# Optimization experiments

Measured on AMD Instinct MI355X. Metric: run time of the kernel, lower is better.

## Reference

```python
import jax, jax.numpy as jnp
import numpy as np

P = 30000      # nodes (WSI patches)
DIN = 1536     # input feature dim
DOUT = 256     # output dim
HEADS = 2
C = DOUT // HEADS  # per-head channels = 128
E = 320000     # edges (before self-loops)
NEG_SLOPE = 0.2


def setup_inputs() -> dict:
    key = jax.random.key(0)
    ks = jax.random.split(key, 12)
    g = lambda k, shape: jax.random.normal(k, shape, jnp.float32) * 0.02
    return {
        "x": jax.random.normal(ks[0], (P, DIN), jnp.float32),
        "edge_index": jax.random.randint(ks[1], (2, E), 0, P),
        "W1l": g(ks[2], (DIN, DOUT)), "b1l": jnp.zeros((DOUT,), jnp.float32),
        "W1r": g(ks[3], (DIN, DOUT)), "b1r": jnp.zeros((DOUT,), jnp.float32),
        "att1": g(ks[4], (HEADS, C)), "bias1": jnp.zeros((DOUT,), jnp.float32),
        "W2l": g(ks[5], (DOUT, DOUT)), "b2l": jnp.zeros((DOUT,), jnp.float32),
        "W2r": g(ks[6], (DOUT, DOUT)), "b2r": jnp.zeros((DOUT,), jnp.float32),
        "att2": g(ks[7], (HEADS, C)), "bias2": jnp.zeros((DOUT,), jnp.float32),
        "ln1_g": jnp.ones((DOUT,), jnp.float32), "ln1_b": jnp.zeros((DOUT,), jnp.float32),
        "ln2_g": jnp.ones((DOUT,), jnp.float32), "ln2_b": jnp.zeros((DOUT,), jnp.float32),
        "resW": g(ks[8], (DIN, DOUT)), "resb": jnp.zeros((DOUT,), jnp.float32),
    }


def layer_norm(h, g, b, eps=1e-5):
    mu = h.mean(-1, keepdims=True)
    var = ((h - mu) ** 2).mean(-1, keepdims=True)
    return (h - mu) * jax.lax.rsqrt(var + eps) * g + b


def gatv2(x, src, dst, Wl, bl, Wr, br, att, bias):
    # PyG GATv2Conv: lin_l on source j, lin_r on target i,
    # e_ij = att . LeakyReLU(xl[j] + xr[i]); softmax over incoming edges of i;
    # out_i = sum_j alpha_ij * xl[j]  (heads concatenated) + bias.
    n = x.shape[0]
    xl = (x @ Wl + bl).reshape(n, HEADS, C)
    xr = (x @ Wr + br).reshape(n, HEADS, C)
    m = jax.nn.leaky_relu(xl[src] + xr[dst], NEG_SLOPE)      # (Etot, H, C)
    e = jnp.einsum('ehc,hc->eh', m, att)                     # (Etot, H)
    emax = jax.ops.segment_max(e, dst, num_segments=n)       # stable segment softmax
    ex = jnp.exp(e - emax[dst])
    den = jax.ops.segment_sum(ex, dst, num_segments=n)
    alpha = ex / den[dst]                                    # (Etot, H)
    out = jax.ops.segment_sum(xl[src] * alpha[..., None], dst, num_segments=n)
    return out.reshape(n, HEADS * C) + bias


def reference(x, edge_index, W1l, b1l, W1r, b1r, att1, bias1,
              W2l, b2l, W2r, b2r, att2, bias2,
              ln1_g, ln1_b, ln2_g, ln2_b, resW, resb):
    loops = jnp.arange(P)
    src = jnp.concatenate([edge_index[0], loops])  # add self loops
    dst = jnp.concatenate([edge_index[1], loops])

    h1 = gatv2(x, src, dst, W1l, b1l, W1r, b1r, att1, bias1)
    h1 = jax.nn.elu(layer_norm(h1, ln1_g, ln1_b)) + (x @ resW + resb)

    h2 = gatv2(h1, src, dst, W2l, b2l, W2r, b2r, att2, bias2)
    h2 = jax.nn.elu(layer_norm(h2, ln2_g, ln2_b)) + h2 * 0 + h1 + (h2 - h1) * 0 if False else jax.nn.elu(layer_norm(h2, ln2_g, ln2_b)) + h1
    # JK-max combine of the two layer outputs
    return jnp.maximum(h1, h2)
```

## Files before the change

### kernel.cpp

```cpp
#include <hip/hip_runtime.h>
#include <math.h>

#define P_NODES 30000
#define DIN_    1536
#define DOUT_   256
#define E_EDGES 320000
#define ET      (E_EDGES + P_NODES)
#define NEG     0.2f

typedef float  f32x4  __attribute__((ext_vector_type(4)));
typedef __bf16 bf16x8 __attribute__((ext_vector_type(8)));
typedef __bf16 bf16x4 __attribute__((ext_vector_type(4)));

__global__ __launch_bounds__(256)
void prep_w1(const float* __restrict__ W1l, const float* __restrict__ W1r,
             const float* __restrict__ resW, __bf16* __restrict__ WT1)
{
    int idx = blockIdx.x * 256 + threadIdx.x;
    if (idx >= DIN_ * 192) return;
    int k = idx / 192;
    int n0 = (idx - k * 192) * 4;
    const float* src; int col;
    if (n0 < 256)      { src = W1l;  col = n0; }
    else if (n0 < 512) { src = W1r;  col = n0 - 256; }
    else               { src = resW; col = n0 - 512; }
    f32x4 v = *(const f32x4*)(src + (size_t)k * DOUT_ + col);
    #pragma unroll
    for (int j = 0; j < 4; ++j)
        WT1[(size_t)(n0 + j) * DIN_ + k] = (__bf16)v[j];
}

__global__ __launch_bounds__(256)
void prep_w2(const float* __restrict__ W2l, const float* __restrict__ W2r,
             __bf16* __restrict__ WT2)
{
    int idx = blockIdx.x * 256 + threadIdx.x;
    if (idx >= 256 * 128) return;
    int k = idx / 128;
    int n0 = (idx - k * 128) * 4;
    const float* src; int col;
    if (n0 < 256) { src = W2l; col = n0; }
    else          { src = W2r; col = n0 - 256; }
    f32x4 v = *(const f32x4*)(src + (size_t)k * DOUT_ + col);
    #pragma unroll
    for (int j = 0; j < 4; ++j)
        WT2[(size_t)(n0 + j) * DOUT_ + k] = (__bf16)v[j];
}

__global__ void prep_bias(const float* b1l, const float* b1r, const float* resb,
                          const float* b2l, const float* b2r,
                          float* B1, float* B2)
{
    int t = threadIdx.x;
    if (t < 256)      B1[t] = b1l[t];
    else if (t < 512) B1[t] = b1r[t - 256];
    else if (t < 768) B1[t] = resb[t - 512];
    if (t < 256)      B2[t] = b2l[t];
    else if (t < 512) B2[t] = b2r[t - 256];
}

__global__ void init_deg(int* deg)
{
    int i = blockIdx.x * 256 + threadIdx.x;
    if (i < P_NODES) deg[i] = 1;
}

__global__ void hist_kernel(const int* __restrict__ dst, int* __restrict__ deg)
{
    int e = blockIdx.x * 256 + threadIdx.x;
    if (e < E_EDGES) atomicAdd(&deg[dst[e]], 1);
}

__global__ __launch_bounds__(1024)
void scan_kernel(const int* __restrict__ deg, int* __restrict__ offs, int* __restrict__ pos)
{
    __shared__ int sb[1024];
    const int t = threadIdx.x;
    const int base = t * 30;
    int ldv[30];
    int lsum = 0;
    #pragma unroll
    for (int i = 0; i < 30; ++i) {
        int idx = base + i;
        int v = (idx < P_NODES) ? deg[idx] : 0;
        ldv[i] = v; lsum += v;
    }
    sb[t] = lsum; __syncthreads();
    for (int off = 1; off < 1024; off <<= 1) {
        int v = (t >= off) ? sb[t - off] : 0;
        __syncthreads();
        sb[t] += v;
        __syncthreads();
    }
    int excl = sb[t] - lsum;
    #pragma unroll
    for (int i = 0; i < 30; ++i) {
        int idx = base + i;
        if (idx < P_NODES) { offs[idx] = excl; pos[idx] = excl; excl += ldv[i]; }
    }
    if (t == 0) offs[P_NODES] = ET;
}

__global__ void scatter_kernel(const int* __restrict__ ei, int* __restrict__ pos,
                               int* __restrict__ srcs)
{
    int tgt = blockIdx.x * 256 + threadIdx.x;
    if (tgt < E_EDGES) {
        int s = ei[tgt];
        int d = ei[E_EDGES + tgt];
        int p = atomicAdd(&pos[d], 1);
        srcs[p] = s;
    } else if (tgt < ET) {
        int i = tgt - E_EDGES;
        int p = atomicAdd(&pos[i], 1);
        srcs[p] = i;
    }
}

template<bool A_F32>
__global__ __launch_bounds__(256)
void gemm_kernel(const void* __restrict__ Av, const __bf16* __restrict__ WT,
                 const float* __restrict__ bias, float* __restrict__ C,
                 int M, int N, int K, int ntiles)
{
    __shared__ __align__(16) __bf16 As[128 * 32];
    __shared__ __align__(16) __bf16 Bs[128 * 32];

    const int bid = blockIdx.x;
    const int mt = bid / ntiles, nt = bid - mt * ntiles;
    const int grow = mt * 128, gcol = nt * 128;
    const int t = threadIdx.x;
    const int lane = t & 63, wave = t >> 6;
    const int wr = wave >> 1, wc = wave & 1;
    const int fr = lane & 15, kg = lane >> 4;

    const int srow = t >> 1, shalf = t & 1;
    int arow = grow + srow; if (arow > M - 1) arow = M - 1;
    const int swz = (srow >> 1) & 3;
    const int g0 = shalf * 2;

    f32x4 acc[4][4] = {};

    for (int k0 = 0; k0 < K; k0 += 32) {
        bf16x8 a0, a1, b0, b1;
        if constexpr (A_F32) {
            const float* ap = (const float*)Av + (size_t)arow * K + k0 + shalf * 16;
            f32x4 v0 = *(const f32x4*)(ap + 0);
            f32x4 v1 = *(const f32x4*)(ap + 4);
            f32x4 v2 = *(const f32x4*)(ap + 8);
            f32x4 v3 = *(const f32x4*)(ap + 12);
            #pragma unroll
            for (int j = 0; j < 4; ++j) {
                a0[j] = (__bf16)v0[j]; a0[j + 4] = (__bf16)v1[j];
                a1[j] = (__bf16)v2[j]; a1[j + 4] = (__bf16)v3[j];
            }
        } else {
            const __bf16* ap = (const __bf16*)Av + (size_t)arow * K + k0 + shalf * 16;
            a0 = *(const bf16x8*)(ap);
            a1 = *(const bf16x8*)(ap + 8);
        }
        {
            const __bf16* bp = WT + (size_t)(gcol + srow) * K + k0 + shalf * 16;
            b0 = *(const bf16x8*)(bp);
            b1 = *(const bf16x8*)(bp + 8);
        }
        __syncthreads();
        *(bf16x8*)&As[srow * 32 + ((g0    ) ^ swz) * 8] = a0;
        *(bf16x8*)&As[srow * 32 + ((g0 + 1) ^ swz) * 8] = a1;
        *(bf16x8*)&Bs[srow * 32 + ((g0    ) ^ swz) * 8] = b0;
        *(bf16x8*)&Bs[srow * 32 + ((g0 + 1) ^ swz) * 8] = b1;
        __syncthreads();

        bf16x8 af[4], bf[4];
        #pragma unroll
        for (int mi = 0; mi < 4; ++mi) {
            int r = wr * 64 + mi * 16 + fr;
            af[mi] = *(const bf16x8*)&As[r * 32 + (kg ^ ((r >> 1) & 3)) * 8];
        }
        #pragma unroll
        for (int ni = 0; ni < 4; ++ni) {
            int r = wc * 64 + ni * 16 + fr;
            bf[ni] = *(const bf16x8*)&Bs[r * 32 + (kg ^ ((r >> 1) & 3)) * 8];
        }
        #pragma unroll
        for (int mi = 0; mi < 4; ++mi)
            #pragma unroll
            for (int ni = 0; ni < 4; ++ni)
                acc[mi][ni] = __builtin_amdgcn_mfma_f32_16x16x32_bf16(af[mi], bf[ni], acc[mi][ni], 0, 0, 0);
    }

    #pragma unroll
    for (int mi = 0; mi < 4; ++mi) {
        #pragma unroll
        for (int ni = 0; ni < 4; ++ni) {
            int col = gcol + wc * 64 + ni * 16 + fr;
            float bv = bias[col];
            #pragma unroll
            for (int j = 0; j < 4; ++j) {
                int row = grow + wr * 64 + mi * 16 + kg * 4 + j;
                if (row < M) C[(size_t)row * N + col] = acc[mi][ni][j] + bv;
            }
        }
    }
}

__global__ __launch_bounds__(256)
void gat_kernel(const float* __restrict__ XLXR, int ld,
                const int* __restrict__ offs, const int* __restrict__ srcs,
                const float* __restrict__ att, const float* __restrict__ bias,
                float* __restrict__ out)
{
    const int node = blockIdx.x * 4 + (threadIdx.x >> 6);
    const int lane = threadIdx.x & 63;
    const int c0 = lane * 4;
    f32x4 xr = *(const f32x4*)(XLXR + (size_t)node * ld + 256 + c0);
    f32x4 at = *(const f32x4*)(att + c0);
    f32x4 acc = {0.f, 0.f, 0.f, 0.f};
    float m = -INFINITY, den = 0.f;
    const int e1 = offs[node + 1];
    for (int e = offs[node]; e < e1; ++e) {
        int s = srcs[e];
        f32x4 xl = *(const f32x4*)(XLXR + (size_t)s * ld + c0);
        float p = 0.f;
        #pragma unroll
        for (int j = 0; j < 4; ++j) {
            float tt = xl[j] + xr[j];
            float lr = tt > 0.f ? tt : NEG * tt;
            p = fmaf(at[j], lr, p);
        }
        #pragma unroll
        for (int w = 1; w < 32; w <<= 1) p += __shfl_xor(p, w, 32);
        float nm = fmaxf(m, p);
        float sc = __expf(m - nm);
        float wv = __expf(p - nm);
        den = den * sc + wv;
        #pragma unroll
        for (int j = 0; j < 4; ++j) acc[j] = acc[j] * sc + wv * xl[j];
        m = nm;
    }
    float inv = 1.f / den;
    f32x4 o;
    #pragma unroll
    for (int j = 0; j < 4; ++j) o[j] = acc[j] * inv + bias[c0 + j];
    *(f32x4*)(out + (size_t)node * DOUT_ + c0) = o;
}

__global__ __launch_bounds__(256)
void h1_kernel(const float* __restrict__ GAT, const float* __restrict__ RESbase, int resld,
               const float* __restrict__ g, const float* __restrict__ b,
               float* __restrict__ H1, __bf16* __restrict__ H1B)
{
    const int node = blockIdx.x * 4 + (threadIdx.x >> 6);
    const int lane = threadIdx.x & 63;
    const int c0 = lane * 4;
    f32x4 h = *(const f32x4*)(GAT + (size_t)node * DOUT_ + c0);
    float s = h[0] + h[1] + h[2] + h[3];
    #pragma unroll
    for (int w = 1; w < 64; w <<= 1) s += __shfl_xor(s, w, 64);
    float mu = s * (1.f / DOUT_);
    f32x4 d; float sq = 0.f;
    #pragma unroll
    for (int j = 0; j < 4; ++j) { d[j] = h[j] - mu; sq += d[j] * d[j]; }
    #pragma unroll
    for (int w = 1; w < 64; w <<= 1) sq += __shfl_xor(sq, w, 64);
    float rs = rsqrtf(sq * (1.f / DOUT_) + 1e-5f);
    f32x4 res = *(const f32x4*)(RESbase + (size_t)node * resld + c0);
    f32x4 o; bf16x4 hb;
    #pragma unroll
    for (int j = 0; j < 4; ++j) {
        float y = d[j] * rs * g[c0 + j] + b[c0 + j];
        float e = y > 0.f ? y : __expf(y) - 1.f;
        o[j] = e + res[j];
        hb[j] = (__bf16)o[j];
    }
    *(f32x4*)(H1 + (size_t)node * DOUT_ + c0) = o;
    *(bf16x4*)(H1B + (size_t)node * DOUT_ + c0) = hb;
}

__global__ __launch_bounds__(256)
void final_kernel(const float* __restrict__ GAT2, const float* __restrict__ H1,
                  const float* __restrict__ g, const float* __restrict__ b,
                  float* __restrict__ out)
{
    const int node = blockIdx.x * 4 + (threadIdx.x >> 6);
    const int lane = threadIdx.x & 63;
    const int c0 = lane * 4;
    f32x4 h = *(const f32x4*)(GAT2 + (size_t)node * DOUT_ + c0);
    float s = h[0] + h[1] + h[2] + h[3];
    #pragma unroll
    for (int w = 1; w < 64; w <<= 1) s += __shfl_xor(s, w, 64);
    float mu = s * (1.f / DOUT_);
    f32x4 d; float sq = 0.f;
    #pragma unroll
    for (int j = 0; j < 4; ++j) { d[j] = h[j] - mu; sq += d[j] * d[j]; }
    #pragma unroll
    for (int w = 1; w < 64; w <<= 1) sq += __shfl_xor(sq, w, 64);
    float rs = rsqrtf(sq * (1.f / DOUT_) + 1e-5f);
    f32x4 h1v = *(const f32x4*)(H1 + (size_t)node * DOUT_ + c0);
    f32x4 o;
    #pragma unroll
    for (int j = 0; j < 4; ++j) {
        float y = d[j] * rs * g[c0 + j] + b[c0 + j];
        float e = y > 0.f ? y : __expf(y) - 1.f;
        float h2 = e + h1v[j];
        o[j] = fmaxf(h1v[j], h2);
    }
    *(f32x4*)(out + (size_t)node * DOUT_ + c0) = o;
}

extern "C" void kernel_launch(void* const* d_in, const int* in_sizes, int n_in,
                              void* d_out, int out_size, void* d_ws, size_t ws_size,
                              hipStream_t stream)
{
    const float* x     = (const float*)d_in[0];
    const int*   ei    = (const int*)d_in[1];
    const float* W1l   = (const float*)d_in[2];
    const float* b1l   = (const float*)d_in[3];
    const float* W1r   = (const float*)d_in[4];
    const float* b1r   = (const float*)d_in[5];
    const float* att1  = (const float*)d_in[6];
    const float* bias1 = (const float*)d_in[7];
    const float* W2l   = (const float*)d_in[8];
    const float* b2l   = (const float*)d_in[9];
    const float* W2r   = (const float*)d_in[10];
    const float* b2r   = (const float*)d_in[11];
    const float* att2  = (const float*)d_in[12];
    const float* bias2 = (const float*)d_in[13];
    const float* ln1g  = (const float*)d_in[14];
    const float* ln1b  = (const float*)d_in[15];
    const float* ln2g  = (const float*)d_in[16];
    const float* ln2b  = (const float*)d_in[17];
    const float* resW  = (const float*)d_in[18];
    const float* resb  = (const float*)d_in[19];
    float* out = (float*)d_out;

    char* w = (char*)d_ws;
    auto alloc = [&](size_t bytes) {
        char* r = w;
        w += (bytes + 255) & ~(size_t)255;
        return r;
    };
    float*  C     = (float*)alloc((size_t)P_NODES * 768 * 4);
    float*  GAT   = (float*)alloc((size_t)P_NODES * 256 * 4);
    float*  H1    = (float*)alloc((size_t)P_NODES * 256 * 4);
    __bf16* H1B   = (__bf16*)alloc((size_t)P_NODES * 256 * 2);
    __bf16* WT1   = (__bf16*)alloc((size_t)768 * DIN_ * 2);
    __bf16* WT2   = (__bf16*)alloc((size_t)512 * DOUT_ * 2);
    float*  BIAS1 = (float*)alloc(768 * 4);
    float*  BIAS2 = (float*)alloc(512 * 4);
    int*    deg   = (int*)alloc((size_t)P_NODES * 4);
    int*    offs  = (int*)alloc((size_t)(P_NODES + 1) * 4);
    int*    pos   = (int*)alloc((size_t)(P_NODES + 1) * 4);
    int*    srcs  = (int*)alloc((size_t)ET * 4);

    prep_w1<<<(DIN_ * 192 + 255) / 256, 256, 0, stream>>>(W1l, W1r, resW, WT1);
    prep_w2<<<(256 * 128 + 255) / 256, 256, 0, stream>>>(W2l, W2r, WT2);
    prep_bias<<<1, 1024, 0, stream>>>(b1l, b1r, resb, b2l, b2r, BIAS1, BIAS2);
    init_deg<<<(P_NODES + 255) / 256, 256, 0, stream>>>(deg);
    hist_kernel<<<(E_EDGES + 255) / 256, 256, 0, stream>>>(ei + E_EDGES, deg);
    scan_kernel<<<1, 1024, 0, stream>>>(deg, offs, pos);
    scatter_kernel<<<(ET + 255) / 256, 256, 0, stream>>>(ei, pos, srcs);

    const int mtiles = (P_NODES + 127) / 128;

    gemm_kernel<true><<<mtiles * 6, 256, 0, stream>>>(x, WT1, BIAS1, C, P_NODES, 768, DIN_, 6);
    gat_kernel<<<P_NODES / 4, 256, 0, stream>>>(C, 768, offs, srcs, att1, bias1, GAT);
    h1_kernel<<<P_NODES / 4, 256, 0, stream>>>(GAT, C + 512, 768, ln1g, ln1b, H1, H1B);

    gemm_kernel<false><<<mtiles * 4, 256, 0, stream>>>(H1B, WT2, BIAS2, C, P_NODES, 512, DOUT_, 4);
    gat_kernel<<<P_NODES / 4, 256, 0, stream>>>(C, 512, offs, srcs, att2, bias2, GAT);
    final_kernel<<<P_NODES / 4, 256, 0, stream>>>(GAT, H1, ln2g, ln2b, out);
}
```

Before: 732.7 us.

## Pre-cast x to swizzled bf16, use direct global-to-LDS loads, store XL/XR in bf16

A separate pass casts x to bf16 in a padded, XOR-swizzled layout, and the weights and H1B are written with the same swizzle. The GEMM can then fill LDS with global_load_lds DMA over a 64-wide K tile and no in-register conversion. The GEMM now writes the XL/XR projections as bf16 and only the residual as fp32, which halves the bytes the gather-heavy GAT kernels read per edge. Costs are an extra full pass over x, lower precision in the attention inputs, and workspace buffers aliased inside the XB region.

```diff
diff --git a/kernel.cpp b/kernel.cpp
--- a/kernel.cpp
+++ b/kernel.cpp
@@ -2,6 +2,7 @@
 #include <math.h>
 
 #define P_NODES 30000
+#define P_PAD   30080
 #define DIN_    1536
 #define DOUT_   256
 #define E_EDGES 320000
@@ -11,6 +12,31 @@
 typedef float  f32x4  __attribute__((ext_vector_type(4)));
 typedef __bf16 bf16x8 __attribute__((ext_vector_type(8)));
 typedef __bf16 bf16x4 __attribute__((ext_vector_type(4)));
+
+__device__ __forceinline__ int swz_col(int c, int row) {
+    return (c & ~63) | ((((c >> 3) ^ row) & 7) << 3) | (c & 7);
+}
+
+__global__ __launch_bounds__(256)
+void cast_x(const float* __restrict__ x, __bf16* __restrict__ XB)
+{
+    int idx = blockIdx.x * 256 + threadIdx.x;
+    if (idx >= P_PAD * 192) return;
+    int row = idx / 192;
+    int c = (idx - row * 192) * 8;
+    int cs = swz_col(c, row);
+    bf16x8 o;
+    if (row < P_NODES) {
+        f32x4 v0 = *(const f32x4*)(x + (size_t)row * DIN_ + c);
+        f32x4 v1 = *(const f32x4*)(x + (size_t)row * DIN_ + c + 4);
+        #pragma unroll
+        for (int j = 0; j < 4; ++j) { o[j] = (__bf16)v0[j]; o[j + 4] = (__bf16)v1[j]; }
+    } else {
+        #pragma unroll
+        for (int j = 0; j < 8; ++j) o[j] = (__bf16)0.f;
+    }
+    *(bf16x8*)(XB + (size_t)row * DIN_ + cs) = o;
+}
 
 __global__ __launch_bounds__(256)
 void prep_w1(const float* __restrict__ W1l, const float* __restrict__ W1r,
@@ -26,8 +52,10 @@
     else               { src = resW; col = n0 - 512; }
     f32x4 v = *(const f32x4*)(src + (size_t)k * DOUT_ + col);
     #pragma unroll
-    for (int j = 0; j < 4; ++j)
-        WT1[(size_t)(n0 + j) * DIN_ + k] = (__bf16)v[j];
+    for (int j = 0; j < 4; ++j) {
+        int n = n0 + j;
+        WT1[(size_t)n * DIN_ + swz_col(k, n)] = (__bf16)v[j];
+    }
 }
 
 __global__ __launch_bounds__(256)
@@ -43,8 +71,10 @@
     else          { src = W2r; col = n0 - 256; }
     f32x4 v = *(const f32x4*)(src + (size_t)k * DOUT_ + col);
     #pragma unroll
-    for (int j = 0; j < 4; ++j)
-        WT2[(size_t)(n0 + j) * DOUT_ + k] = (__bf16)v[j];
+    for (int j = 0; j < 4; ++j) {
+        int n = n0 + j;
+        WT2[(size_t)n * DOUT_ + swz_col(k, n)] = (__bf16)v[j];
+    }
 }
 
 __global__ void prep_bias(const float* b1l, const float* b1r, const float* resb,
@@ -117,14 +147,15 @@
     }
 }
 
-template<bool A_F32>
-__global__ __launch_bounds__(256)
-void gemm_kernel(const void* __restrict__ Av, const __bf16* __restrict__ WT,
-                 const float* __restrict__ bias, float* __restrict__ C,
+template<int EPI>
+__global__ __launch_bounds__(256)
+void gemm_kernel(const __bf16* __restrict__ A, const __bf16* __restrict__ WT,
+                 const float* __restrict__ bias,
+                 __bf16* __restrict__ Cb, float* __restrict__ Cf,
                  int M, int N, int K, int ntiles)
 {
-    __shared__ __align__(16) __bf16 As[128 * 32];
-    __shared__ __align__(16) __bf16 Bs[128 * 32];
+    __shared__ __align__(16) __bf16 As[128 * 64];
+    __shared__ __align__(16) __bf16 Bs[128 * 64];
 
     const int bid = blockIdx.x;
     const int mt = bid / ntiles, nt = bid - mt * ntiles;
@@ -133,60 +164,44 @@
     const int lane = t & 63, wave = t >> 6;
     const int wr = wave >> 1, wc = wave & 1;
     const int fr = lane & 15, kg = lane >> 4;
-
-    const int srow = t >> 1, shalf = t & 1;
-    int arow = grow + srow; if (arow > M - 1) arow = M - 1;
-    const int swz = (srow >> 1) & 3;
-    const int g0 = shalf * 2;
+    const int frs = fr & 7;
+
+    const __bf16* agp = A  + (size_t)(grow + (t >> 3)) * K + (t & 7) * 8;
+    const __bf16* bgp = WT + (size_t)(gcol + (t >> 3)) * K + (t & 7) * 8;
+    const size_t rstep = (size_t)32 * K;
+    char* lA = (char*)As + wave * 1024;
+    char* lB = (char*)Bs + wave * 1024;
 
     f32x4 acc[4][4] = {};
 
-    for (int k0 = 0; k0 < K; k0 += 32) {
-        bf16x8 a0, a1, b0, b1;
-        if constexpr (A_F32) {
-            const float* ap = (const float*)Av + (size_t)arow * K + k0 + shalf * 16;
-            f32x4 v0 = *(const f32x4*)(ap + 0);
-            f32x4 v1 = *(const f32x4*)(ap + 4);
-            f32x4 v2 = *(const f32x4*)(ap + 8);
-            f32x4 v3 = *(const f32x4*)(ap + 12);
-            #pragma unroll
-            for (int j = 0; j < 4; ++j) {
-                a0[j] = (__bf16)v0[j]; a0[j + 4] = (__bf16)v1[j];
-                a1[j] = (__bf16)v2[j]; a1[j + 4] = (__bf16)v3[j];
-            }
-        } else {
-            const __bf16* ap = (const __bf16*)Av + (size_t)arow * K + k0 + shalf * 16;
-            a0 = *(const bf16x8*)(ap);
-            a1 = *(const bf16x8*)(ap + 8);
-        }
-        {
-            const __bf16* bp = WT + (size_t)(gcol + srow) * K + k0 + shalf * 16;
-            b0 = *(const bf16x8*)(bp);
-            b1 = *(const bf16x8*)(bp + 8);
+    for (int k0 = 0; k0 < K; k0 += 64) {
+        __syncthreads();
+        #pragma unroll
+        for (int i = 0; i < 4; ++i) {
+            __builtin_amdgcn_global_load_lds(
+                (const __attribute__((address_space(1))) void*)(agp + i * rstep + k0),
+                (__attribute__((address_space(3))) void*)(lA + i * 4096), 16, 0, 0);
+            __builtin_amdgcn_global_load_lds(
+                (const __attribute__((address_space(1))) void*)(bgp + i * rstep + k0),
+                (__attribute__((address_space(3))) void*)(lB + i * 4096), 16, 0, 0);
         }
         __syncthreads();
-        *(bf16x8*)&As[srow * 32 + ((g0    ) ^ swz) * 8] = a0;
-        *(bf16x8*)&As[srow * 32 + ((g0 + 1) ^ swz) * 8] = a1;
-        *(bf16x8*)&Bs[srow * 32 + ((g0    ) ^ swz) * 8] = b0;
-        *(bf16x8*)&Bs[srow * 32 + ((g0 + 1) ^ swz) * 8] = b1;
-        __syncthreads();
-
-        bf16x8 af[4], bf[4];
-        #pragma unroll
-        for (int mi = 0; mi < 4; ++mi) {
-            int r = wr * 64 + mi * 16 + fr;
-            af[mi] = *(const bf16x8*)&As[r * 32 + (kg ^ ((r >> 1) & 3)) * 8];
-        }
-        #pragma unroll
-        for (int ni = 0; ni < 4; ++ni) {
-            int r = wc * 64 + ni * 16 + fr;
-            bf[ni] = *(const bf16x8*)&Bs[r * 32 + (kg ^ ((r >> 1) & 3)) * 8];
-        }
-        #pragma unroll
-        for (int mi = 0; mi < 4; ++mi)
+
+        #pragma unroll
+        for (int ks = 0; ks < 2; ++ks) {
+            bf16x8 af[4], bv[4];
+            #pragma unroll
+            for (int mi = 0; mi < 4; ++mi)
+                af[mi] = *(const bf16x8*)&As[(wr * 64 + mi * 16 + fr) * 64 + (((ks * 4 + kg) ^ frs)) * 8];
             #pragma unroll
             for (int ni = 0; ni < 4; ++ni)
-                acc[mi][ni] = __builtin_amdgcn_mfma_f32_16x16x32_bf16(af[mi], bf[ni], acc[mi][ni], 0, 0, 0);
+                bv[ni] = *(const bf16x8*)&Bs[(wc * 64 + ni * 16 + fr) * 64 + (((ks * 4 + kg) ^ frs)) * 8];
+            #pragma unroll
+            for (int mi = 0; mi < 4; ++mi)
+                #pragma unroll
+                for (int ni = 0; ni < 4; ++ni)
+                    acc[mi][ni] = __builtin_amdgcn_mfma_f32_16x16x32_bf16(af[mi], bv[ni], acc[mi][ni], 0, 0, 0);
+        }
     }
 
     #pragma unroll
@@ -194,18 +209,26 @@
         #pragma unroll
         for (int ni = 0; ni < 4; ++ni) {
             int col = gcol + wc * 64 + ni * 16 + fr;
-            float bv = bias[col];
+            float bvv = bias[col];
             #pragma unroll
             for (int j = 0; j < 4; ++j) {
                 int row = grow + wr * 64 + mi * 16 + kg * 4 + j;
-                if (row < M) C[(size_t)row * N + col] = acc[mi][ni][j] + bv;
+                if (row < M) {
+                    float v = acc[mi][ni][j] + bvv;
+                    if (EPI == 0) {
+                        if (col < 512) Cb[(size_t)row * 512 + col] = (__bf16)v;
+                        else           Cf[(size_t)row * 256 + col - 512] = v;
+                    } else {
+                        Cb[(size_t)row * 512 + col] = (__bf16)v;
+                    }
+                }
             }
         }
     }
 }
 
 __global__ __launch_bounds__(256)
-void gat_kernel(const float* __restrict__ XLXR, int ld,
+void gat_kernel(const __bf16* __restrict__ XLXR,
                 const int* __restrict__ offs, const int* __restrict__ srcs,
                 const float* __restrict__ att, const float* __restrict__ bias,
                 float* __restrict__ out)
@@ -213,17 +236,21 @@
     const int node = blockIdx.x * 4 + (threadIdx.x >> 6);
     const int lane = threadIdx.x & 63;
     const int c0 = lane * 4;
-    f32x4 xr = *(const f32x4*)(XLXR + (size_t)node * ld + 256 + c0);
-    f32x4 at = *(const f32x4*)(att + c0);
+    bf16x4 xrb = *(const bf16x4*)(XLXR + (size_t)node * 512 + 256 + c0);
+    f32x4 xr, at = *(const f32x4*)(att + c0);
+    #pragma unroll
+    for (int j = 0; j < 4; ++j) xr[j] = (float)xrb[j];
     f32x4 acc = {0.f, 0.f, 0.f, 0.f};
     float m = -INFINITY, den = 0.f;
     const int e1 = offs[node + 1];
     for (int e = offs[node]; e < e1; ++e) {
         int s = srcs[e];
-        f32x4 xl = *(const f32x4*)(XLXR + (size_t)s * ld + c0);
+        bf16x4 xlb = *(const bf16x4*)(XLXR + (size_t)s * 512 + c0);
+        f32x4 xl;
         float p = 0.f;
         #pragma unroll
         for (int j = 0; j < 4; ++j) {
+            xl[j] = (float)xlb[j];
             float tt = xl[j] + xr[j];
             float lr = tt > 0.f ? tt : NEG * tt;
             p = fmaf(at[j], lr, p);
@@ -246,13 +273,21 @@
 }
 
 __global__ __launch_bounds__(256)
-void h1_kernel(const float* __restrict__ GAT, const float* __restrict__ RESbase, int resld,
+void h1_kernel(const float* __restrict__ GAT, const float* __restrict__ RES,
                const float* __restrict__ g, const float* __restrict__ b,
                float* __restrict__ H1, __bf16* __restrict__ H1B)
 {
     const int node = blockIdx.x * 4 + (threadIdx.x >> 6);
     const int lane = threadIdx.x & 63;
     const int c0 = lane * 4;
+    const int cs = swz_col(c0, node);
+    if (node >= P_NODES) {
+        bf16x4 z; 
+        #pragma unroll
+        for (int j = 0; j < 4; ++j) z[j] = (__bf16)0.f;
+        *(bf16x4*)(H1B + (size_t)node * DOUT_ + cs) = z;
+        return;
+    }
     f32x4 h = *(const f32x4*)(GAT + (size_t)node * DOUT_ + c0);
     float s = h[0] + h[1] + h[2] + h[3];
     #pragma unroll
@@ -264,7 +299,7 @@
     #pragma unroll
     for (int w = 1; w < 64; w <<= 1) sq += __shfl_xor(sq, w, 64);
     float rs = rsqrtf(sq * (1.f / DOUT_) + 1e-5f);
-    f32x4 res = *(const f32x4*)(RESbase + (size_t)node * resld + c0);
+    f32x4 res = *(const f32x4*)(RES + (size_t)node * DOUT_ + c0);
     f32x4 o; bf16x4 hb;
     #pragma unroll
     for (int j = 0; j < 4; ++j) {
@@ -274,7 +309,7 @@
         hb[j] = (__bf16)o[j];
     }
     *(f32x4*)(H1 + (size_t)node * DOUT_ + c0) = o;
-    *(bf16x4*)(H1B + (size_t)node * DOUT_ + c0) = hb;
+    *(bf16x4*)(H1B + (size_t)node * DOUT_ + cs) = hb;
 }
 
 __global__ __launch_bounds__(256)
@@ -340,10 +375,10 @@
         w += (bytes + 255) & ~(size_t)255;
         return r;
     };
-    float*  C     = (float*)alloc((size_t)P_NODES * 768 * 4);
-    float*  GAT   = (float*)alloc((size_t)P_NODES * 256 * 4);
+    __bf16* XB    = (__bf16*)alloc((size_t)P_PAD * DIN_ * 2);
+    __bf16* XLR1  = (__bf16*)alloc((size_t)P_NODES * 512 * 2);
+    float*  RES   = (float*)alloc((size_t)P_NODES * 256 * 4);
     float*  H1    = (float*)alloc((size_t)P_NODES * 256 * 4);
-    __bf16* H1B   = (__bf16*)alloc((size_t)P_NODES * 256 * 2);
     __bf16* WT1   = (__bf16*)alloc((size_t)768 * DIN_ * 2);
     __bf16* WT2   = (__bf16*)alloc((size_t)512 * DOUT_ * 2);
     float*  BIAS1 = (float*)alloc(768 * 4);
@@ -353,6 +388,11 @@
     int*    pos   = (int*)alloc((size_t)(P_NODES + 1) * 4);
     int*    srcs  = (int*)alloc((size_t)ET * 4);
 
+    __bf16* XLR2 = (__bf16*)XB;
+    __bf16* H1B  = (__bf16*)((char*)XB + (size_t)32 * 1024 * 1024);
+    float*  GAT  = (float*)((char*)XB + (size_t)48 * 1024 * 1024);
+
+    cast_x<<<(P_PAD * 192 + 255) / 256, 256, 0, stream>>>(x, XB);
     prep_w1<<<(DIN_ * 192 + 255) / 256, 256, 0, stream>>>(W1l, W1r, resW, WT1);
     prep_w2<<<(256 * 128 + 255) / 256, 256, 0, stream>>>(W2l, W2r, WT2);
     prep_bias<<<1, 1024, 0, stream>>>(b1l, b1r, resb, b2l, b2r, BIAS1, BIAS2);
@@ -361,13 +401,13 @@
     scan_kernel<<<1, 1024, 0, stream>>>(deg, offs, pos);
     scatter_kernel<<<(ET + 255) / 256, 256, 0, stream>>>(ei, pos, srcs);
 
-    const int mtiles = (P_NODES + 127) / 128;
-
-    gemm_kernel<true><<<mtiles * 6, 256, 0, stream>>>(x, WT1, BIAS1, C, P_NODES, 768, DIN_, 6);
-    gat_kernel<<<P_NODES / 4, 256, 0, stream>>>(C, 768, offs, srcs, att1, bias1, GAT);
-    h1_kernel<<<P_NODES / 4, 256, 0, stream>>>(GAT, C + 512, 768, ln1g, ln1b, H1, H1B);
-
-    gemm_kernel<false><<<mtiles * 4, 256, 0, stream>>>(H1B, WT2, BIAS2, C, P_NODES, 512, DOUT_, 4);
-    gat_kernel<<<P_NODES / 4, 256, 0, stream>>>(C, 512, offs, srcs, att2, bias2, GAT);
+    const int mtiles = P_PAD / 128;
+
+    gemm_kernel<0><<<mtiles * 6, 256, 0, stream>>>(XB, WT1, BIAS1, XLR1, RES, P_NODES, 768, DIN_, 6);
+    gat_kernel<<<P_NODES / 4, 256, 0, stream>>>(XLR1, offs, srcs, att1, bias1, GAT);
+    h1_kernel<<<P_PAD / 4, 256, 0, stream>>>(GAT, RES, ln1g, ln1b, H1, H1B);
+
+    gemm_kernel<1><<<mtiles * 4, 256, 0, stream>>>(H1B, WT2, BIAS2, XLR2, nullptr, P_NODES, 512, DOUT_, 4);
+    gat_kernel<<<P_NODES / 4, 256, 0, stream>>>(XLR2, offs, srcs, att2, bias2, GAT);
     final_kernel<<<P_NODES / 4, 256, 0, stream>>>(GAT, H1, ln2g, ln2b, out);
 }
```

Measured after the change: 659.7 us. -10.0%, faster.
